# Performance work log

Measured on AMD Instinct MI355X. Metric: run time of the kernel, lower is better.

The kernel has to match this reference:

```python
import jax, jax.numpy as jnp
import numpy as np

K = 9          # kernel taps along the space-filling curve
SIGMA = 1.0    # gaussian bandwidth (conv2 uses SIGMA * stride, stride=1)
EPS = 1e-5     # BatchNorm eps


def _weighted_conv(x, w, coords, indices, reindices, sigma):
    """Gather points into curve order, run a k-tap 1D conv whose taps are
    modulated by a Gaussian of coordinate distance, scatter back.
    x: [B,C,N], w: [O,C,K], coords: [B,3,N], indices/reindices: [B,N]."""
    B, C, N = x.shape
    pad = K // 2
    idx = indices[:, None, :]
    xp = jnp.take_along_axis(x, jnp.broadcast_to(idx, (B, C, N)), axis=2)        # curve order
    cp = jnp.take_along_axis(coords, jnp.broadcast_to(idx, (B, 3, N)), axis=2)
    x_pad = jnp.pad(xp, ((0, 0), (0, 0), (pad, pad)))
    c_pad = jnp.pad(cp, ((0, 0), (0, 0), (pad, pad)))
    inv_s2 = 1.0 / (sigma * sigma)
    out = jnp.zeros((B, w.shape[0], N), x.dtype)
    for t in range(K):  # small fixed loop over kernel taps
        xw = x_pad[:, :, t:t + N]                     # [B,C,N]
        rel = c_pad[:, :, t:t + N] - cp               # [B,3,N]
        g = jnp.exp(-jnp.sum(rel * rel, axis=1) * inv_s2)  # [B,N] gaussian weight
        out = out + jnp.einsum('oc,bcn->bon', w[:, :, t], xw * g[:, None, :])
    ridx = reindices[:, None, :]
    return jnp.take_along_axis(out, jnp.broadcast_to(ridx, out.shape), axis=2)


def _batchnorm1d(x, gamma, beta):
    # training-mode BN over (batch, points) per channel, biased variance
    mean = jnp.mean(x, axis=(0, 2), keepdims=True)
    var = jnp.mean((x - mean) ** 2, axis=(0, 2), keepdims=True)
    return gamma[None, :, None] * (x - mean) * jax.lax.rsqrt(var + EPS) + beta[None, :, None]


def setup_inputs() -> dict:
    key = jax.random.key(0)
    ks = jax.random.split(key, 6)
    B, C, N = 4, 128, 65536
    x = jax.random.normal(ks[0], (B, C, N), jnp.float32)
    coords = jax.random.uniform(ks[1], (B, 3, N), jnp.float32)
    perm = jnp.stack([jax.random.permutation(jax.random.fold_in(ks[2], b), N) for b in range(B)])
    indices = perm.astype(jnp.int32)
    reindices = jnp.argsort(perm, axis=1).astype(jnp.int32)
    w1 = jax.random.normal(ks[3], (C, C, K), jnp.float32) * 0.05
    w2 = jax.random.normal(ks[4], (C, C, K), jnp.float32) * 0.05
    gamma1 = jnp.ones((C,), jnp.float32)
    beta1 = jnp.zeros((C,), jnp.float32)
    gamma2 = jnp.ones((C,), jnp.float32)
    beta2 = jnp.zeros((C,), jnp.float32)
    return {"x": x, "coords": coords, "indices": indices, "reindices": reindices,
            "w1": w1, "gamma1": gamma1, "beta1": beta1,
            "w2": w2, "gamma2": gamma2, "beta2": beta2}


def reference(x, coords, indices, reindices, w1, gamma1, beta1, w2, gamma2, beta2):
    identity = x
    out = _weighted_conv(x, w1, coords, indices, reindices, SIGMA)
    out = jax.nn.relu(_batchnorm1d(out, gamma1, beta1))
    out = _weighted_conv(out, w2, coords, indices, reindices, SIGMA * 1)  # stride=1
    out = _batchnorm1d(out, gamma2, beta2)
    return jax.nn.relu(out + identity)
```

## Files before the change

### kernel.cpp

```cpp
#include <hip/hip_runtime.h>

#define Bn 4
#define Cn 128
#define Nn 65536
#define KT 9
#define T_OUT 256
#define T_HALO 264
#define XROW 136
#define GROW 264
#define FT 66

typedef _Float16 f16x8 __attribute__((ext_vector_type(8)));
typedef _Float16 f16x4 __attribute__((ext_vector_type(4)));
typedef float f32x4 __attribute__((ext_vector_type(4)));
typedef float f32x2 __attribute__((ext_vector_type(2)));

__global__ __launch_bounds__(256) void repack_w(const float* __restrict__ w1,
                                                const float* __restrict__ w2,
                                                _Float16* __restrict__ Wr) {
  int i = blockIdx.x * 256 + threadIdx.x;
  int c = i & 127;
  int o = (i >> 7) & 127;
  int t = (i >> 14) % KT;
  int cv = i / (KT << 14);
  const float* w = cv ? w2 : w1;
  Wr[i] = (_Float16)w[(o * 128 + c) * KT + t];
}

__global__ __launch_bounds__(256) void gather_x(const float* __restrict__ x,
                                                const int* __restrict__ reidx,
                                                _Float16* __restrict__ xp) {
  __shared__ float ft[128 * FT];
  int tid = threadIdx.x;
  int b = blockIdx.x >> 10;
  int n0 = (blockIdx.x & 1023) * 64;
  const float* xb = x + (size_t)b * Cn * Nn;
  {
    int cc = tid >> 4;
    int j4 = (tid & 15) * 4;
#pragma unroll
    for (int pass = 0; pass < 8; ++pass) {
      int c = pass * 16 + cc;
      f32x4 v = *(const f32x4*)(&xb[(size_t)c * Nn + n0 + j4]);
      *(f32x2*)(&ft[c * FT + j4]) = f32x2{v.x, v.y};
      *(f32x2*)(&ft[c * FT + j4 + 2]) = f32x2{v.z, v.w};
    }
  }
  __syncthreads();
  int ch = tid & 15;
  int rr = tid >> 4;
#pragma unroll
  for (int pass = 0; pass < 4; ++pass) {
    int r = pass * 16 + rr;
    int m = reidx[(size_t)b * Nn + n0 + r];
    f16x8 v;
#pragma unroll
    for (int k = 0; k < 8; ++k) v[k] = (_Float16)ft[(ch * 8 + k) * FT + r];
    *(f16x8*)(xp + ((size_t)b * Nn + m) * Cn + ch * 8) = v;
  }
}

__global__ __launch_bounds__(256) void gather_cp(const float* __restrict__ coords,
                                                 const int* __restrict__ indices,
                                                 float* __restrict__ cp) {
  int gidx = blockIdx.x * 256 + threadIdx.x;
  int b = gidx >> 16;
  int m = gidx & (Nn - 1);
  int idx = indices[gidx];
  const float* cb = coords + (size_t)b * 3 * Nn;
  float* cpb = cp + (size_t)b * 3 * Nn;
  cpb[m] = cb[idx];
  cpb[Nn + m] = cb[Nn + idx];
  cpb[2 * Nn + m] = cb[2 * Nn + idx];
}

__global__ __launch_bounds__(256) void compute_g(const float* __restrict__ cp,
                                                 float* __restrict__ G) {
  int gidx = blockIdx.x * 256 + threadIdx.x;
  int b = gidx >> 16;
  int m = gidx & (Nn - 1);
  const float* cpb = cp + (size_t)b * 3 * Nn;
  float x0 = cpb[m], y0 = cpb[Nn + m], z0 = cpb[2 * Nn + m];
  float* Gb = G + (size_t)b * KT * Nn;
#pragma unroll
  for (int t = 0; t < KT; ++t) {
    int q = m + t - 4;
    q = q < 0 ? 0 : (q > Nn - 1 ? Nn - 1 : q);
    float dx = cpb[q] - x0;
    float dy = cpb[Nn + q] - y0;
    float dz = cpb[2 * Nn + q] - z0;
    Gb[(size_t)t * Nn + m] = __expf(-(dx * dx + dy * dy + dz * dz));
  }
}

__global__ void bncoeff(const float* __restrict__ sums,
                        const float* __restrict__ gamma,
                        const float* __restrict__ beta,
                        float* __restrict__ coeff) {
  int c = threadIdx.x;
  const float inv = 1.0f / (float)((size_t)Bn * Nn);
  float mean = sums[c] * inv;
  float var = sums[128 + c] * inv - mean * mean;
  float a = gamma[c] * rsqrtf(var + 1e-5f);
  coeff[c] = a;
  coeff[128 + c] = beta[c] - mean * a;
}

__device__ __forceinline__ f16x8 scale8(f16x8 v, _Float16 g) {
  f16x8 r;
#pragma unroll
  for (int i = 0; i < 8; ++i) r[i] = v[i] * g;
  return r;
}

template <int TRANS>
__global__ __launch_bounds__(256, 2) void conv_mfma(
    const _Float16* __restrict__ Xin, const _Float16* __restrict__ W,
    const float* __restrict__ G, _Float16* __restrict__ Yout,
    float* __restrict__ sums, const float* __restrict__ coeff) {
  __shared__ __align__(16) _Float16 Xs[T_HALO * XROW];
  __shared__ __align__(16) unsigned char aux[KT * GROW * 2];
  _Float16* Gs = (_Float16*)aux;
  float* red = (float*)aux;

  const int tid = threadIdx.x;
  const int b = blockIdx.x >> 8;
  const int p0 = (blockIdx.x & 255) * T_OUT;
  const int ch = tid & 15;

#pragma unroll
  for (int pass = 0; pass < 17; ++pass) {
    int r = pass * 16 + (tid >> 4);
    if (r < T_HALO) {
      int q = p0 - 4 + r;
      f16x8 v = {0, 0, 0, 0, 0, 0, 0, 0};
      if (q >= 0 && q < Nn) {
        v = *(const f16x8*)(Xin + ((size_t)b * Nn + q) * Cn + ch * 8);
        if (TRANS) {
#pragma unroll
          for (int i = 0; i < 8; ++i) {
            float f = fmaxf(coeff[ch * 8 + i] * (float)v[i] + coeff[128 + ch * 8 + i], 0.f);
            v[i] = (_Float16)f;
          }
        }
      }
      *(f16x8*)(&Xs[r * XROW + ch * 8]) = v;
    }
  }
  {
    const float* gb = G + (size_t)b * KT * Nn + p0;
    for (int i = tid; i < KT * 256; i += 256) {
      int t = i >> 8;
      int p = i & 255;
      Gs[t * GROW + p] = (_Float16)gb[(size_t)t * Nn + p];
    }
  }

  const int w = tid >> 6;
  const int lane = tid & 63;
  const int l15 = lane & 15;
  const int quad = lane >> 4;
  const int wm = w >> 1;
  const int wn = w & 1;

  f32x4 acc[4][8];
  const f32x4 z4 = {0.f, 0.f, 0.f, 0.f};
#pragma unroll
  for (int mt = 0; mt < 4; ++mt)
#pragma unroll
    for (int nt = 0; nt < 8; ++nt) acc[mt][nt] = z4;

  __syncthreads();

#pragma unroll 1
  for (int t = 0; t < KT; ++t) {
    _Float16 gt[8];
#pragma unroll
    for (int nt = 0; nt < 8; ++nt)
      gt[nt] = Gs[t * GROW + wn * 128 + nt * 16 + l15];

    const _Float16* Wt = W + ((size_t)t << 14) + (wm * 64) * Cn;
#pragma unroll
    for (int ko = 0; ko < 4; ++ko) {
      f16x8 a[4];
#pragma unroll
      for (int mt = 0; mt < 4; ++mt)
        a[mt] = *(const f16x8*)(Wt + (mt * 16 + l15) * Cn + ko * 32 + quad * 8);
#pragma unroll
      for (int nt = 0; nt < 8; ++nt) {
        f16x8 bv = *(const f16x8*)(&Xs[(wn * 128 + nt * 16 + l15 + t) * XROW + ko * 32 + quad * 8]);
        bv = scale8(bv, gt[nt]);
#pragma unroll
        for (int mt = 0; mt < 4; ++mt)
          acc[mt][nt] = __builtin_amdgcn_mfma_f32_16x16x32_f16(a[mt], bv, acc[mt][nt], 0, 0, 0);
      }
    }
  }

  f32x4 s4[4], q4[4];
#pragma unroll
  for (int mt = 0; mt < 4; ++mt) {
#pragma unroll
    for (int rg = 0; rg < 4; ++rg) {
      float s = 0.f, q = 0.f;
#pragma unroll
      for (int nt = 0; nt < 8; ++nt) {
        float v = acc[mt][nt][rg];
        s += v;
        q += v * v;
      }
#pragma unroll
      for (int m = 1; m < 16; m <<= 1) {
        s += __shfl_xor(s, m);
        q += __shfl_xor(q, m);
      }
      s4[mt][rg] = s;
      q4[mt][rg] = q;
    }
  }
  __syncthreads();
  if (l15 == 0) {
#pragma unroll
    for (int mt = 0; mt < 4; ++mt) {
      int cbase = wm * 64 + mt * 16 + quad * 4;
      *(f32x4*)(&red[wn * 128 + cbase]) = s4[mt];
      *(f32x4*)(&red[256 + wn * 128 + cbase]) = q4[mt];
    }
  }

  _Float16* Os = Xs;
#pragma unroll
  for (int mt = 0; mt < 4; ++mt)
#pragma unroll
    for (int nt = 0; nt < 8; ++nt) {
      f16x4 o4;
#pragma unroll
      for (int rg = 0; rg < 4; ++rg) o4[rg] = (_Float16)acc[mt][nt][rg];
      *(f16x4*)(&Os[(wn * 128 + nt * 16 + l15) * XROW + wm * 64 + mt * 16 + quad * 4]) = o4;
    }
  __syncthreads();

  if (tid < 128) {
    atomicAdd(&sums[tid], red[tid] + red[128 + tid]);
    atomicAdd(&sums[128 + tid], red[256 + tid] + red[384 + tid]);
  }
#pragma unroll
  for (int pass = 0; pass < 16; ++pass) {
    int r = pass * 16 + (tid >> 4);
    f16x8 v = *(const f16x8*)(&Os[r * XROW + ch * 8]);
    *(f16x8*)(Yout + ((size_t)b * Nn + p0 + r) * Cn + ch * 8) = v;
  }
}

__global__ __launch_bounds__(256) void final_k(const _Float16* __restrict__ y2,
                                               const float* __restrict__ x,
                                               const int* __restrict__ reidx,
                                               const float* __restrict__ coeff,
                                               float* __restrict__ out) {
  __shared__ float ft[128 * FT];
  int tid = threadIdx.x;
  int b = blockIdx.x >> 10;
  int n0 = (blockIdx.x & 1023) * 64;
  {
    int ch = tid & 15;
#pragma unroll
    for (int pass = 0; pass < 4; ++pass) {
      int r = pass * 16 + (tid >> 4);
      int m = reidx[(size_t)b * Nn + n0 + r];
      f16x8 v = *(const f16x8*)(y2 + ((size_t)b * Nn + m) * Cn + ch * 8);
#pragma unroll
      for (int k = 0; k < 8; ++k) ft[(ch * 8 + k) * FT + r] = (float)v[k];
    }
  }
  __syncthreads();
  int cc = tid >> 4;
  int j4 = (tid & 15) * 4;
#pragma unroll
  for (int pass = 0; pass < 8; ++pass) {
    int c = pass * 16 + cc;
    float a = coeff[c];
    float bb = coeff[128 + c];
    f32x2 v0 = *(const f32x2*)(&ft[c * FT + j4]);
    f32x2 v1 = *(const f32x2*)(&ft[c * FT + j4 + 2]);
    size_t gi = ((size_t)b * Cn + c) * Nn + n0 + j4;
    f32x4 xv = *(const f32x4*)(&x[gi]);
    f32x4 r;
    r.x = fmaxf(a * v0.x + bb + xv.x, 0.f);
    r.y = fmaxf(a * v0.y + bb + xv.y, 0.f);
    r.z = fmaxf(a * v1.x + bb + xv.z, 0.f);
    r.w = fmaxf(a * v1.y + bb + xv.w, 0.f);
    *(f32x4*)(&out[gi]) = r;
  }
}

extern "C" void kernel_launch(void* const* d_in, const int* in_sizes, int n_in,
                              void* d_out, int out_size, void* d_ws, size_t ws_size,
                              hipStream_t stream) {
  (void)in_sizes; (void)n_in; (void)out_size; (void)ws_size;
  const float* x = (const float*)d_in[0];
  const float* coords = (const float*)d_in[1];
  const int* indices = (const int*)d_in[2];
  const int* reindices = (const int*)d_in[3];
  const float* w1 = (const float*)d_in[4];
  const float* gamma1 = (const float*)d_in[5];
  const float* beta1 = (const float*)d_in[6];
  const float* w2 = (const float*)d_in[7];
  const float* gamma2 = (const float*)d_in[8];
  const float* beta2 = (const float*)d_in[9];
  float* out = (float*)d_out;

  char* ws = (char*)d_ws;
  const size_t BUF0 = (size_t)Bn * Nn * Cn * sizeof(_Float16);
  _Float16* buf0 = (_Float16*)ws;
  float* sums1 = (float*)(ws + BUF0);
  float* sums2 = sums1 + 256;
  float* coeff1 = sums1 + 512;
  float* coeff2 = sums1 + 768;
  _Float16* Wr = (_Float16*)(ws + BUF0 + 4096);

  char* dob = (char*)d_out;
  _Float16* y1 = (_Float16*)dob;
  float* cp = (float*)(dob + BUF0);
  float* G = (float*)(dob + BUF0 + (size_t)Bn * 3 * Nn * 4);

  hipMemsetAsync(sums1, 0, 512 * sizeof(float), stream);

  repack_w<<<1152, 256, 0, stream>>>(w1, w2, Wr);
  gather_x<<<Bn * 1024, 256, 0, stream>>>(x, reindices, buf0);
  gather_cp<<<1024, 256, 0, stream>>>(coords, indices, cp);
  compute_g<<<1024, 256, 0, stream>>>(cp, G);

  conv_mfma<0><<<Bn * 256, 256, 0, stream>>>(buf0, Wr, G, y1, sums1, nullptr);
  bncoeff<<<1, 128, 0, stream>>>(sums1, gamma1, beta1, coeff1);
  conv_mfma<1><<<Bn * 256, 256, 0, stream>>>(y1, Wr + (size_t)KT * Cn * Cn, G,
                                             buf0, sums2, coeff1);
  bncoeff<<<1, 128, 0, stream>>>(sums2, gamma2, beta2, coeff2);
  final_k<<<Bn * 1024, 256, 0, stream>>>(buf0, x, reindices, coeff2, out);
}
```

Measured before the change: 563.4 us.

## Fuse coordinate gather with gaussian weights and use 8-wave conv for layer one

Merges gather_cp and compute_g into one kernel that stages the gathered coordinates plus halo in shared memory, which removes the intermediate cp buffer and one launch. Adds conv_mfma8, a 512-thread variant of the first conv where each wave owns a 64x64 output tile, cutting per-thread accumulators so more waves fit per CU. The extra waves trade fewer registers per thread for more W loads from global memory and a wider block-level reduction.

```diff
diff --git a/kernel.cpp b/kernel.cpp
--- a/kernel.cpp
+++ b/kernel.cpp
@@ -60,35 +60,31 @@
   }
 }
 
-__global__ __launch_bounds__(256) void gather_cp(const float* __restrict__ coords,
-                                                 const int* __restrict__ indices,
-                                                 float* __restrict__ cp) {
-  int gidx = blockIdx.x * 256 + threadIdx.x;
-  int b = gidx >> 16;
-  int m = gidx & (Nn - 1);
-  int idx = indices[gidx];
+__global__ __launch_bounds__(256) void gather_g(const float* __restrict__ coords,
+                                                const int* __restrict__ indices,
+                                                float* __restrict__ G) {
+  __shared__ float cx[264], cy[264], cz[264];
+  int tid = threadIdx.x;
+  int b = blockIdx.x >> 8;
+  int n0 = (blockIdx.x & 255) * 256;
   const float* cb = coords + (size_t)b * 3 * Nn;
-  float* cpb = cp + (size_t)b * 3 * Nn;
-  cpb[m] = cb[idx];
-  cpb[Nn + m] = cb[Nn + idx];
-  cpb[2 * Nn + m] = cb[2 * Nn + idx];
-}
-
-__global__ __launch_bounds__(256) void compute_g(const float* __restrict__ cp,
-                                                 float* __restrict__ G) {
-  int gidx = blockIdx.x * 256 + threadIdx.x;
-  int b = gidx >> 16;
-  int m = gidx & (Nn - 1);
-  const float* cpb = cp + (size_t)b * 3 * Nn;
-  float x0 = cpb[m], y0 = cpb[Nn + m], z0 = cpb[2 * Nn + m];
+  for (int i = tid; i < 264; i += 256) {
+    int q = n0 - 4 + i;
+    q = q < 0 ? 0 : (q > Nn - 1 ? Nn - 1 : q);
+    int idx = indices[(size_t)b * Nn + q];
+    cx[i] = cb[idx];
+    cy[i] = cb[Nn + idx];
+    cz[i] = cb[2 * Nn + idx];
+  }
+  __syncthreads();
+  int m = n0 + tid;
+  float x0 = cx[tid + 4], y0 = cy[tid + 4], z0 = cz[tid + 4];
   float* Gb = G + (size_t)b * KT * Nn;
 #pragma unroll
   for (int t = 0; t < KT; ++t) {
-    int q = m + t - 4;
-    q = q < 0 ? 0 : (q > Nn - 1 ? Nn - 1 : q);
-    float dx = cpb[q] - x0;
-    float dy = cpb[Nn + q] - y0;
-    float dz = cpb[2 * Nn + q] - z0;
+    float dx = cx[tid + t] - x0;
+    float dy = cy[tid + t] - y0;
+    float dz = cz[tid + t] - z0;
     Gb[(size_t)t * Nn + m] = __expf(-(dx * dx + dy * dy + dz * dz));
   }
 }
@@ -247,6 +243,138 @@
 #pragma unroll
   for (int pass = 0; pass < 16; ++pass) {
     int r = pass * 16 + (tid >> 4);
+    f16x8 v = *(const f16x8*)(&Os[r * XROW + ch * 8]);
+    *(f16x8*)(Yout + ((size_t)b * Nn + p0 + r) * Cn + ch * 8) = v;
+  }
+}
+
+__global__ __launch_bounds__(512, 4) void conv_mfma8(
+    const _Float16* __restrict__ Xin, const _Float16* __restrict__ W,
+    const float* __restrict__ G, _Float16* __restrict__ Yout,
+    float* __restrict__ sums) {
+  __shared__ __align__(16) _Float16 Xs[T_HALO * XROW];
+  __shared__ __align__(16) unsigned char aux[KT * GROW * 2];
+  _Float16* Gs = (_Float16*)aux;
+  float* red = (float*)aux;
+
+  const int tid = threadIdx.x;
+  const int b = blockIdx.x >> 8;
+  const int p0 = (blockIdx.x & 255) * T_OUT;
+  const int ch = tid & 15;
+
+#pragma unroll
+  for (int pass = 0; pass < 9; ++pass) {
+    int r = pass * 32 + (tid >> 4);
+    if (r < T_HALO) {
+      int q = p0 - 4 + r;
+      f16x8 v = {0, 0, 0, 0, 0, 0, 0, 0};
+      if (q >= 0 && q < Nn)
+        v = *(const f16x8*)(Xin + ((size_t)b * Nn + q) * Cn + ch * 8);
+      *(f16x8*)(&Xs[r * XROW + ch * 8]) = v;
+    }
+  }
+  {
+    const float* gb = G + (size_t)b * KT * Nn + p0;
+    for (int i = tid; i < KT * 256; i += 512) {
+      int t = i >> 8;
+      int p = i & 255;
+      Gs[t * GROW + p] = (_Float16)gb[(size_t)t * Nn + p];
+    }
+  }
+
+  const int w = tid >> 6;
+  const int lane = tid & 63;
+  const int l15 = lane & 15;
+  const int quad = lane >> 4;
+  const int wm = w >> 2;
+  const int wn = w & 3;
+
+  f32x4 acc[4][4];
+  const f32x4 z4 = {0.f, 0.f, 0.f, 0.f};
+#pragma unroll
+  for (int mt = 0; mt < 4; ++mt)
+#pragma unroll
+    for (int nt = 0; nt < 4; ++nt) acc[mt][nt] = z4;
+
+  __syncthreads();
+
+#pragma unroll 1
+  for (int t = 0; t < KT; ++t) {
+    _Float16 gt[4];
+#pragma unroll
+    for (int nt = 0; nt < 4; ++nt)
+      gt[nt] = Gs[t * GROW + wn * 64 + nt * 16 + l15];
+
+    const _Float16* Wt = W + ((size_t)t << 14) + (wm * 64) * Cn;
+#pragma unroll
+    for (int ko = 0; ko < 4; ++ko) {
+      f16x8 a4[4];
+#pragma unroll
+      for (int mt = 0; mt < 4; ++mt)
+        a4[mt] = *(const f16x8*)(Wt + (mt * 16 + l15) * Cn + ko * 32 + quad * 8);
+#pragma unroll
+      for (int nt = 0; nt < 4; ++nt) {
+        f16x8 bv = *(const f16x8*)(&Xs[(wn * 64 + nt * 16 + l15 + t) * XROW + ko * 32 + quad * 8]);
+        bv = scale8(bv, gt[nt]);
+#pragma unroll
+        for (int mt = 0; mt < 4; ++mt)
+          acc[mt][nt] = __builtin_amdgcn_mfma_f32_16x16x32_f16(a4[mt], bv, acc[mt][nt], 0, 0, 0);
+      }
+    }
+  }
+
+  f32x4 s4[4], q4[4];
+#pragma unroll
+  for (int mt = 0; mt < 4; ++mt) {
+#pragma unroll
+    for (int rg = 0; rg < 4; ++rg) {
+      float s = 0.f, q = 0.f;
+#pragma unroll
+      for (int nt = 0; nt < 4; ++nt) {
+        float v = acc[mt][nt][rg];
+        s += v;
+        q += v * v;
+      }
+#pragma unroll
+      for (int m = 1; m < 16; m <<= 1) {
+        s += __shfl_xor(s, m);
+        q += __shfl_xor(q, m);
+      }
+      s4[mt][rg] = s;
+      q4[mt][rg] = q;
+    }
+  }
+  __syncthreads();
+  if (l15 == 0) {
+#pragma unroll
+    for (int mt = 0; mt < 4; ++mt) {
+      int cbase = wm * 64 + mt * 16 + quad * 4;
+      *(f32x4*)(&red[wn * 128 + cbase]) = s4[mt];
+      *(f32x4*)(&red[512 + wn * 128 + cbase]) = q4[mt];
+    }
+  }
+
+  _Float16* Os = Xs;
+#pragma unroll
+  for (int mt = 0; mt < 4; ++mt)
+#pragma unroll
+    for (int nt = 0; nt < 4; ++nt) {
+      f16x4 o4;
+#pragma unroll
+      for (int rg = 0; rg < 4; ++rg) o4[rg] = (_Float16)acc[mt][nt][rg];
+      *(f16x4*)(&Os[(wn * 64 + nt * 16 + l15) * XROW + wm * 64 + mt * 16 + quad * 4]) = o4;
+    }
+  __syncthreads();
+
+  if (tid < 128) {
+    atomicAdd(&sums[tid],
+              red[tid] + red[128 + tid] + red[256 + tid] + red[384 + tid]);
+    atomicAdd(&sums[128 + tid],
+              red[512 + tid] + red[640 + tid] + red[768 + tid] + red[896 + tid]);
+  }
+#pragma unroll
+  for (int pass = 0; pass < 8; ++pass) {
+    int r = pass * 32 + (tid >> 4);
     f16x8 v = *(const f16x8*)(&Os[r * XROW + ch * 8]);
     *(f16x8*)(Yout + ((size_t)b * Nn + p0 + r) * Cn + ch * 8) = v;
   }
@@ -320,17 +448,15 @@
 
   char* dob = (char*)d_out;
   _Float16* y1 = (_Float16*)dob;
-  float* cp = (float*)(dob + BUF0);
-  float* G = (float*)(dob + BUF0 + (size_t)Bn * 3 * Nn * 4);
+  float* G = (float*)(dob + BUF0);
 
   hipMemsetAsync(sums1, 0, 512 * sizeof(float), stream);
 
   repack_w<<<1152, 256, 0, stream>>>(w1, w2, Wr);
   gather_x<<<Bn * 1024, 256, 0, stream>>>(x, reindices, buf0);
-  gather_cp<<<1024, 256, 0, stream>>>(coords, indices, cp);
-  compute_g<<<1024, 256, 0, stream>>>(cp, G);
-
-  conv_mfma<0><<<Bn * 256, 256, 0, stream>>>(buf0, Wr, G, y1, sums1, nullptr);
+  gather_g<<<Bn * 256, 256, 0, stream>>>(coords, indices, G);
+
+  conv_mfma8<<<Bn * 256, 512, 0, stream>>>(buf0, Wr, G, y1, sums1);
   bncoeff<<<1, 128, 0, stream>>>(sums1, gamma1, beta1, coeff1);
   conv_mfma<1><<<Bn * 256, 256, 0, stream>>>(y1, Wr + (size_t)KT * Cn * Cn, G,
                                              buf0, sums2, coeff1);
```

Measured after the change: 616.7 us. +9.5%, slower.

## Stage conv weights in double-buffered LDS with 512-thread blocks; fuse gather/gaussian

Applied to the files above, without the earlier changes.

The conv kernel now uses 512 threads (8 waves, each owning 32 output channels instead of 64). Per-tap weights are double-buffered in LDS and prefetched two taps ahead into registers, where before each wave read them straight from global memory. The coordinate gather and gaussian-weight kernels are merged into one that stages curve-ordered coords in shared memory, removing the intermediate cp buffer. This cuts global weight traffic and register pressure per thread, at the cost of much larger LDS use (about 70KB for Xs plus 2x34KB of weights) and a barrier every tap, which may limit occupancy to one block per CU.

```diff
diff --git a/kernel.cpp b/kernel.cpp
--- a/kernel.cpp
+++ b/kernel.cpp
@@ -60,35 +60,31 @@
   }
 }
 
-__global__ __launch_bounds__(256) void gather_cp(const float* __restrict__ coords,
-                                                 const int* __restrict__ indices,
-                                                 float* __restrict__ cp) {
-  int gidx = blockIdx.x * 256 + threadIdx.x;
-  int b = gidx >> 16;
-  int m = gidx & (Nn - 1);
-  int idx = indices[gidx];
+__global__ __launch_bounds__(256) void gather_g(const float* __restrict__ coords,
+                                                const int* __restrict__ indices,
+                                                float* __restrict__ G) {
+  __shared__ float cx[264], cy[264], cz[264];
+  int tid = threadIdx.x;
+  int b = blockIdx.x >> 8;
+  int n0 = (blockIdx.x & 255) * 256;
   const float* cb = coords + (size_t)b * 3 * Nn;
-  float* cpb = cp + (size_t)b * 3 * Nn;
-  cpb[m] = cb[idx];
-  cpb[Nn + m] = cb[Nn + idx];
-  cpb[2 * Nn + m] = cb[2 * Nn + idx];
-}
-
-__global__ __launch_bounds__(256) void compute_g(const float* __restrict__ cp,
-                                                 float* __restrict__ G) {
-  int gidx = blockIdx.x * 256 + threadIdx.x;
-  int b = gidx >> 16;
-  int m = gidx & (Nn - 1);
-  const float* cpb = cp + (size_t)b * 3 * Nn;
-  float x0 = cpb[m], y0 = cpb[Nn + m], z0 = cpb[2 * Nn + m];
+  for (int i = tid; i < 264; i += 256) {
+    int q = n0 - 4 + i;
+    q = q < 0 ? 0 : (q > Nn - 1 ? Nn - 1 : q);
+    int idx = indices[(size_t)b * Nn + q];
+    cx[i] = cb[idx];
+    cy[i] = cb[Nn + idx];
+    cz[i] = cb[2 * Nn + idx];
+  }
+  __syncthreads();
+  int m = n0 + tid;
+  float x0 = cx[tid + 4], y0 = cy[tid + 4], z0 = cz[tid + 4];
   float* Gb = G + (size_t)b * KT * Nn;
 #pragma unroll
   for (int t = 0; t < KT; ++t) {
-    int q = m + t - 4;
-    q = q < 0 ? 0 : (q > Nn - 1 ? Nn - 1 : q);
-    float dx = cpb[q] - x0;
-    float dy = cpb[Nn + q] - y0;
-    float dz = cpb[2 * Nn + q] - z0;
+    float dx = cx[tid + t] - x0;
+    float dy = cy[tid + t] - y0;
+    float dz = cz[tid + t] - z0;
     Gb[(size_t)t * Nn + m] = __expf(-(dx * dx + dy * dy + dz * dz));
   }
 }
@@ -114,11 +110,12 @@
 }
 
 template <int TRANS>
-__global__ __launch_bounds__(256, 2) void conv_mfma(
+__global__ __launch_bounds__(512) void conv_wlds(
     const _Float16* __restrict__ Xin, const _Float16* __restrict__ W,
     const float* __restrict__ G, _Float16* __restrict__ Yout,
     float* __restrict__ sums, const float* __restrict__ coeff) {
   __shared__ __align__(16) _Float16 Xs[T_HALO * XROW];
+  __shared__ __align__(16) _Float16 Wlds[2][128 * XROW];
   __shared__ __align__(16) unsigned char aux[KT * GROW * 2];
   _Float16* Gs = (_Float16*)aux;
   float* red = (float*)aux;
@@ -128,9 +125,17 @@
   const int p0 = (blockIdx.x & 255) * T_OUT;
   const int ch = tid & 15;
 
-#pragma unroll
-  for (int pass = 0; pass < 17; ++pass) {
-    int r = pass * 16 + (tid >> 4);
+  f16x8 w0r[4], w1r[4];
+#pragma unroll
+  for (int i = 0; i < 4; ++i) {
+    int q = i * 512 + tid;
+    w0r[i] = *(const f16x8*)(W + (q >> 4) * 128 + (q & 15) * 8);
+    w1r[i] = *(const f16x8*)(W + 16384 + (q >> 4) * 128 + (q & 15) * 8);
+  }
+
+#pragma unroll
+  for (int pass = 0; pass < 9; ++pass) {
+    int r = pass * 32 + (tid >> 4);
     if (r < T_HALO) {
       int q = p0 - 4 + r;
       f16x8 v = {0, 0, 0, 0, 0, 0, 0, 0};
@@ -149,11 +154,17 @@
   }
   {
     const float* gb = G + (size_t)b * KT * Nn + p0;
-    for (int i = tid; i < KT * 256; i += 256) {
+    for (int i = tid; i < KT * 256; i += 512) {
       int t = i >> 8;
       int p = i & 255;
       Gs[t * GROW + p] = (_Float16)gb[(size_t)t * Nn + p];
     }
+  }
+#pragma unroll
+  for (int i = 0; i < 4; ++i) {
+    int q = i * 512 + tid;
+    *(f16x8*)(&Wlds[0][(q >> 4) * XROW + (q & 15) * 8]) = w0r[i];
+    *(f16x8*)(&Wlds[1][(q >> 4) * XROW + (q & 15) * 8]) = w1r[i];
   }
 
   const int w = tid >> 6;
@@ -163,43 +174,62 @@
   const int wm = w >> 1;
   const int wn = w & 1;
 
-  f32x4 acc[4][8];
+  f32x4 acc[2][8];
   const f32x4 z4 = {0.f, 0.f, 0.f, 0.f};
 #pragma unroll
-  for (int mt = 0; mt < 4; ++mt)
+  for (int mt = 0; mt < 2; ++mt)
 #pragma unroll
     for (int nt = 0; nt < 8; ++nt) acc[mt][nt] = z4;
 
   __syncthreads();
 
+  f16x8 wpre[4];
 #pragma unroll 1
   for (int t = 0; t < KT; ++t) {
+    if (t <= KT - 3) {
+      const _Float16* Wt2 = W + ((size_t)(t + 2) << 14);
+#pragma unroll
+      for (int i = 0; i < 4; ++i) {
+        int q = i * 512 + tid;
+        wpre[i] = *(const f16x8*)(Wt2 + (q >> 4) * 128 + (q & 15) * 8);
+      }
+    }
+
     _Float16 gt[8];
 #pragma unroll
     for (int nt = 0; nt < 8; ++nt)
       gt[nt] = Gs[t * GROW + wn * 128 + nt * 16 + l15];
 
-    const _Float16* Wt = W + ((size_t)t << 14) + (wm * 64) * Cn;
+    const _Float16* Wb = &Wlds[t & 1][0];
 #pragma unroll
     for (int ko = 0; ko < 4; ++ko) {
-      f16x8 a[4];
-#pragma unroll
-      for (int mt = 0; mt < 4; ++mt)
-        a[mt] = *(const f16x8*)(Wt + (mt * 16 + l15) * Cn + ko * 32 + quad * 8);
+      f16x8 a2[2];
+#pragma unroll
+      for (int mt = 0; mt < 2; ++mt)
+        a2[mt] = *(const f16x8*)(Wb + (wm * 32 + mt * 16 + l15) * XROW + ko * 32 + quad * 8);
 #pragma unroll
       for (int nt = 0; nt < 8; ++nt) {
         f16x8 bv = *(const f16x8*)(&Xs[(wn * 128 + nt * 16 + l15 + t) * XROW + ko * 32 + quad * 8]);
         bv = scale8(bv, gt[nt]);
 #pragma unroll
-        for (int mt = 0; mt < 4; ++mt)
-          acc[mt][nt] = __builtin_amdgcn_mfma_f32_16x16x32_f16(a[mt], bv, acc[mt][nt], 0, 0, 0);
-      }
-    }
-  }
-
-  f32x4 s4[4], q4[4];
-#pragma unroll
-  for (int mt = 0; mt < 4; ++mt) {
+        for (int mt = 0; mt < 2; ++mt)
+          acc[mt][nt] = __builtin_amdgcn_mfma_f32_16x16x32_f16(a2[mt], bv, acc[mt][nt], 0, 0, 0);
+      }
+    }
+
+    __syncthreads();
+    if (t <= KT - 3) {
+#pragma unroll
+      for (int i = 0; i < 4; ++i) {
+        int q = i * 512 + tid;
+        *(f16x8*)(&Wlds[t & 1][(q >> 4) * XROW + (q & 15) * 8]) = wpre[i];
+      }
+    }
+  }
+
+  f32x4 s4[2], q4[2];
+#pragma unroll
+  for (int mt = 0; mt < 2; ++mt) {
 #pragma unroll
     for (int rg = 0; rg < 4; ++rg) {
       float s = 0.f, q = 0.f;
@@ -218,11 +248,10 @@
       q4[mt][rg] = q;
     }
   }
-  __syncthreads();
   if (l15 == 0) {
 #pragma unroll
-    for (int mt = 0; mt < 4; ++mt) {
-      int cbase = wm * 64 + mt * 16 + quad * 4;
+    for (int mt = 0; mt < 2; ++mt) {
+      int cbase = wm * 32 + mt * 16 + quad * 4;
       *(f32x4*)(&red[wn * 128 + cbase]) = s4[mt];
       *(f32x4*)(&red[256 + wn * 128 + cbase]) = q4[mt];
     }
@@ -230,13 +259,13 @@
 
   _Float16* Os = Xs;
 #pragma unroll
-  for (int mt = 0; mt < 4; ++mt)
+  for (int mt = 0; mt < 2; ++mt)
 #pragma unroll
     for (int nt = 0; nt < 8; ++nt) {
       f16x4 o4;
 #pragma unroll
       for (int rg = 0; rg < 4; ++rg) o4[rg] = (_Float16)acc[mt][nt][rg];
-      *(f16x4*)(&Os[(wn * 128 + nt * 16 + l15) * XROW + wm * 64 + mt * 16 + quad * 4]) = o4;
+      *(f16x4*)(&Os[(wn * 128 + nt * 16 + l15) * XROW + wm * 32 + mt * 16 + quad * 4]) = o4;
     }
   __syncthreads();
 
@@ -245,8 +274,8 @@
     atomicAdd(&sums[128 + tid], red[256 + tid] + red[384 + tid]);
   }
 #pragma unroll
-  for (int pass = 0; pass < 16; ++pass) {
-    int r = pass * 16 + (tid >> 4);
+  for (int pass = 0; pass < 8; ++pass) {
+    int r = pass * 32 + (tid >> 4);
     f16x8 v = *(const f16x8*)(&Os[r * XROW + ch * 8]);
     *(f16x8*)(Yout + ((size_t)b * Nn + p0 + r) * Cn + ch * 8) = v;
   }
@@ -320,19 +349,17 @@
 
   char* dob = (char*)d_out;
   _Float16* y1 = (_Float16*)dob;
-  float* cp = (float*)(dob + BUF0);
-  float* G = (float*)(dob + BUF0 + (size_t)Bn * 3 * Nn * 4);
+  float* G = (float*)(dob + BUF0);
 
   hipMemsetAsync(sums1, 0, 512 * sizeof(float), stream);
 
   repack_w<<<1152, 256, 0, stream>>>(w1, w2, Wr);
   gather_x<<<Bn * 1024, 256, 0, stream>>>(x, reindices, buf0);
-  gather_cp<<<1024, 256, 0, stream>>>(coords, indices, cp);
-  compute_g<<<1024, 256, 0, stream>>>(cp, G);
-
-  conv_mfma<0><<<Bn * 256, 256, 0, stream>>>(buf0, Wr, G, y1, sums1, nullptr);
+  gather_g<<<Bn * 256, 256, 0, stream>>>(coords, indices, G);
+
+  conv_wlds<0><<<Bn * 256, 512, 0, stream>>>(buf0, Wr, G, y1, sums1, nullptr);
   bncoeff<<<1, 128, 0, stream>>>(sums1, gamma1, beta1, coeff1);
-  conv_mfma<1><<<Bn * 256, 256, 0, stream>>>(y1, Wr + (size_t)KT * Cn * Cn, G,
+  conv_wlds<1><<<Bn * 256, 512, 0, stream>>>(y1, Wr + (size_t)KT * Cn * Cn, G,
                                              buf0, sums2, coeff1);
   bncoeff<<<1, 128, 0, stream>>>(sums2, gamma2, beta2, coeff2);
   final_k<<<Bn * 1024, 256, 0, stream>>>(buf0, x, reindices, coeff2, out);
```

After: 524.2 us. 7.0% less time.
